# Kernel optimization log

Hardware: AMD Instinct MI355X
Metric: run time of the kernel (lower is better)

## Reference

```python
import jax, jax.numpy as jnp
import numpy as np

N = 320
C_Z = 128
H = 4
C_H = 32


def setup_inputs() -> dict:
    key = jax.random.key(0)
    ks = jax.random.split(key, 9)
    s = 0.02
    return {
        "x_normed": jax.random.normal(ks[0], (1, N, N, C_Z), dtype=jnp.float32),
        "triangle_bias": jax.random.normal(ks[1], (1, 1, H, N, N), dtype=jnp.float32),
        "wq": jax.random.normal(ks[2], (C_Z, H * C_H), dtype=jnp.float32) * s,
        "wk": jax.random.normal(ks[3], (C_Z, H * C_H), dtype=jnp.float32) * s,
        "wv": jax.random.normal(ks[4], (C_Z, H * C_H), dtype=jnp.float32) * s,
        "wg": jax.random.normal(ks[5], (C_Z, H * C_H), dtype=jnp.float32) * s,
        "bg": jnp.ones((H * C_H,), dtype=jnp.float32),  # OpenFold gating bias init = 1
        "wo": jax.random.normal(ks[6], (H * C_H, C_Z), dtype=jnp.float32) * s,
        "bo": jnp.zeros((C_Z,), dtype=jnp.float32),
    }


def reference(x_normed, triangle_bias, wq, wk, wv, wg, bg, wo, bo):
    b, n, m, cz = x_normed.shape  # [1, N, N, C_Z]
    # q/k/v projections (no bias, per OpenFold Attention)
    q = (x_normed @ wq).reshape(b, n, m, H, C_H) / np.sqrt(C_H)
    k = (x_normed @ wk).reshape(b, n, m, H, C_H)
    v = (x_normed @ wv).reshape(b, n, m, H, C_H)
    # attention over the last row dim; first N is a batch dim.
    # scores: [b, n, H, q, k]; triangle_bias [1, 1, H, N, N] broadcasts over n.
    scores = jnp.einsum("bnqhc,bnkhc->bnhqk", q, k) + triangle_bias
    a = jax.nn.softmax(scores, axis=-1)
    o = jnp.einsum("bnhqk,bnkhc->bnqhc", a, v)
    # sigmoid output gating
    g = jax.nn.sigmoid((x_normed @ wg + bg).reshape(b, n, m, H, C_H))
    o = o * g
    out = o.reshape(b, n, m, H * C_H) @ wo + bo
    return out
```

## Files before the change

kernel.cpp:

```cpp
#include <hip/hip_runtime.h>

typedef __bf16 bf16;
typedef __bf16 bf16x8 __attribute__((ext_vector_type(8)));
typedef __bf16 bf16x4 __attribute__((ext_vector_type(4)));
typedef __bf16 bf16x2 __attribute__((ext_vector_type(2)));
typedef float  f32x4  __attribute__((ext_vector_type(4)));
typedef unsigned int u32;
typedef u32 u32x4 __attribute__((ext_vector_type(4)));

#define NN_  320
#define CZ_  128
#define H_   4
#define CH_  32
#define LOG2E_ 1.4426950408889634f

__device__ __forceinline__ u32 pack_bf16(float a, float b) {
    bf16x2 t; t[0] = (bf16)a; t[1] = (bf16)b;
    return __builtin_bit_cast(u32, t);
}

__global__ __launch_bounds__(512) void qkvg_kernel(
    const float* __restrict__ x,
    const float* __restrict__ wq, const float* __restrict__ wk,
    const float* __restrict__ wv, const float* __restrict__ wg,
    const float* __restrict__ bg,
    bf16* __restrict__ Qp, bf16* __restrict__ Kp,
    bf16* __restrict__ Vp, bf16* __restrict__ Gp)
{
    __shared__ bf16 wl[128][136];
    const int tid  = threadIdx.x;
    const int lane = tid & 63, wid = tid >> 6;
    const int l15  = lane & 15, l4 = lane >> 4;
    const int m0   = blockIdx.x << 7;

    const int arow = m0 + wid * 16 + l15;
    bf16x8 xf[4];
    #pragma unroll
    for (int ks = 0; ks < 4; ++ks) {
        float4 f0 = *reinterpret_cast<const float4*>(x + (size_t)arow * CZ_ + ks * 32 + l4 * 8);
        float4 f1 = *reinterpret_cast<const float4*>(x + (size_t)arow * CZ_ + ks * 32 + l4 * 8 + 4);
        bf16x8 t;
        t[0]=(bf16)f0.x; t[1]=(bf16)f0.y; t[2]=(bf16)f0.z; t[3]=(bf16)f0.w;
        t[4]=(bf16)f1.x; t[5]=(bf16)f1.y; t[6]=(bf16)f1.z; t[7]=(bf16)f1.w;
        xf[ks] = t;
    }

    int nQ[4], qQ[4];
    #pragma unroll
    for (int r = 0; r < 4; ++r) {
        int m = m0 + wid * 16 + l4 * 4 + r;
        nQ[r] = m / NN_; qQ[r] = m - nQ[r] * NN_;
    }
    const int nV = arow / NN_, qV = arow - nV * NN_;

    const float* Ws[4] = {wq, wk, wv, wg};
    #pragma unroll
    for (int mat = 0; mat < 4; ++mat) {
        __syncthreads();
        const float* w = Ws[mat];
        #pragma unroll
        for (int it = 0; it < 8; ++it) {
            int u  = tid + (it << 9);
            int j  = u & 127, k4 = u >> 7;
            bf16x4 t;
            t[0] = (bf16)w[(k4 * 4 + 0) * CZ_ + j];
            t[1] = (bf16)w[(k4 * 4 + 1) * CZ_ + j];
            t[2] = (bf16)w[(k4 * 4 + 2) * CZ_ + j];
            t[3] = (bf16)w[(k4 * 4 + 3) * CZ_ + j];
            *reinterpret_cast<bf16x4*>(&wl[j][k4 * 4]) = t;
        }
        __syncthreads();

        f32x4 zero = {0.f, 0.f, 0.f, 0.f};
        f32x4 acc[8];
        #pragma unroll
        for (int ct = 0; ct < 8; ++ct) acc[ct] = zero;

        #pragma unroll
        for (int ks = 0; ks < 4; ++ks) {
            #pragma unroll
            for (int ct = 0; ct < 8; ++ct) {
                bf16x8 wf = *reinterpret_cast<const bf16x8*>(&wl[ct * 16 + l15][ks * 32 + l4 * 8]);
                if (mat == 2)
                    acc[ct] = __builtin_amdgcn_mfma_f32_16x16x32_bf16(wf, xf[ks], acc[ct], 0, 0, 0);
                else
                    acc[ct] = __builtin_amdgcn_mfma_f32_16x16x32_bf16(xf[ks], wf, acc[ct], 0, 0, 0);
            }
        }

        if (mat == 0) {
            #pragma unroll
            for (int ct = 0; ct < 8; ++ct) {
                const int cout = ct * 16 + l15, hh = cout >> 5, cc = cout & 31;
                #pragma unroll
                for (int r = 0; r < 4; ++r)
                    Qp[(size_t)((nQ[r] * H_ + hh) * NN_ + qQ[r]) * CH_ + cc] =
                        (bf16)(acc[ct][r] * 0.25500003540695464f);
            }
        } else if (mat == 1) {
            #pragma unroll
            for (int ct = 0; ct < 8; ++ct) {
                const int cout = ct * 16 + l15, hh = cout >> 5, cc = cout & 31;
                #pragma unroll
                for (int r = 0; r < 4; ++r)
                    Kp[(size_t)((nQ[r] * H_ + hh) * NN_ + qQ[r]) * CH_ + cc] = (bf16)acc[ct][r];
            }
        } else if (mat == 2) {
            #pragma unroll
            for (int ct = 0; ct < 8; ++ct) {
                #pragma unroll
                for (int r = 0; r < 4; ++r) {
                    const int cout = ct * 16 + l4 * 4 + r, hh = cout >> 5, cc = cout & 31;
                    Vp[(size_t)((nV * H_ + hh) * CH_ + cc) * NN_ + qV] = (bf16)acc[ct][r];
                }
            }
        } else {
            #pragma unroll
            for (int ct = 0; ct < 8; ++ct) {
                const int cout = ct * 16 + l15;
                const float bgj = bg[cout];
                #pragma unroll
                for (int r = 0; r < 4; ++r) {
                    float t = acc[ct][r] + bgj;
                    Gp[(size_t)(m0 + wid * 16 + l4 * 4 + r) * CZ_ + cout] =
                        (bf16)(1.0f / (1.0f + __expf(-t)));
                }
            }
        }
    }
}

__global__ __launch_bounds__(640, 3) void attn_kernel(
    const bf16* __restrict__ Qp, const bf16* __restrict__ Kp,
    const bf16* __restrict__ Vp, bf16* __restrict__ Gp,
    const float* __restrict__ bias)
{
    __shared__ bf16 Kl[320][40];
    __shared__ bf16 Vl[32][328];
    const int tid  = threadIdx.x;
    const int lane = tid & 63;
    const int wid  = tid >> 6;
    const int l15  = lane & 15, l4 = lane >> 4;
    const int gid = blockIdx.x;
    const int lin = (gid & 7) * 160 + (gid >> 3);
    const int h   = lin / NN_;
    const int n   = lin - h * NN_;

    const size_t nh = (size_t)(n * H_ + h);
    const bf16* Kh = Kp + nh * NN_ * CH_;
    const bf16* Vh = Vp + nh * CH_ * NN_;
    const bf16* Qh = Qp + nh * NN_ * CH_;

    #pragma unroll
    for (int i = 0; i < 2; ++i) {
        int c  = tid + i * 640;
        int kr = c >> 2, kc = (c & 3) * 8;
        *reinterpret_cast<bf16x8*>(&Kl[kr][kc]) =
            *reinterpret_cast<const bf16x8*>(Kh + kr * CH_ + kc);
        int vr = c / 40, vc = c - vr * 40;
        int m = vc & 3, b32 = vc >> 2;
        bf16x8 g = *reinterpret_cast<const bf16x8*>(Vh + vr * NN_ + vc * 8);
        int base = b32 * 32 + (m & 1) * 16 + (m >> 1) * 4;
        bf16x4 lo; lo[0] = g[0]; lo[1] = g[1]; lo[2] = g[2]; lo[3] = g[3];
        bf16x4 hi; hi[0] = g[4]; hi[1] = g[5]; hi[2] = g[6]; hi[3] = g[7];
        *reinterpret_cast<bf16x4*>(&Vl[vr][base]) = lo;
        *reinterpret_cast<bf16x4*>(&Vl[vr][base + 8]) = hi;
    }
    __syncthreads();

    const f32x4 zero = {0.f, 0.f, 0.f, 0.f};
    bf16x8 onesf;
    #pragma unroll
    for (int i = 0; i < 8; ++i) onesf[i] = (bf16)1.0f;

    const int qbq[2] = {wid * 32, wid * 32 + 16};
    bf16x8 qf[2];
    const float* bq[2];
    size_t gbase[2];
    bf16x4 g0[2], g1[2];
    f32x4 o0[2], o1[2], ol[2];
    float4 bA0[2], bA1[2], bB0[2], bB1[2];

    #pragma unroll
    for (int qg = 0; qg < 2; ++qg) {
        const int qb = qbq[qg];
        qf[qg] = *reinterpret_cast<const bf16x8*>(&Qh[(qb + l15) * CH_ + l4 * 8]);
        bq[qg] = bias + ((size_t)h * NN_ + qb + l15) * NN_ + l4 * 4;
        gbase[qg] = ((size_t)n * NN_ + qb + l15) * CZ_ + h * CH_;
        g0[qg] = *reinterpret_cast<const bf16x4*>(&Gp[gbase[qg] + l4 * 4]);
        g1[qg] = *reinterpret_cast<const bf16x4*>(&Gp[gbase[qg] + 16 + l4 * 4]);
        o0[qg] = zero; o1[qg] = zero; ol[qg] = zero;
        bA0[qg] = *reinterpret_cast<const float4*>(bq[qg]);
        bA1[qg] = *reinterpret_cast<const float4*>(bq[qg] + 16);
        bB0[qg] = *reinterpret_cast<const float4*>(bq[qg] + 32);
        bB1[qg] = *reinterpret_cast<const float4*>(bq[qg] + 48);
    }

#define ATTN_TP(TP, B0, B1, PRE)                                                   \
    {                                                                              \
        const int kvm = (TP) * 32;                                                 \
        bf16x8 kf0 = *reinterpret_cast<const bf16x8*>(&Kl[kvm + l15][l4 * 8]);     \
        bf16x8 kf1 = *reinterpret_cast<const bf16x8*>(&Kl[kvm + 16 + l15][l4 * 8]);\
        bf16x8 vf0 = *reinterpret_cast<const bf16x8*>(&Vl[l15][kvm + l4 * 8]);     \
        bf16x8 vf1 = *reinterpret_cast<const bf16x8*>(&Vl[16 + l15][kvm + l4 * 8]);\
        f32x4 s0[2], s1[2];                                                        \
        __builtin_amdgcn_s_setprio(1);                                             \
        s0[0] = __builtin_amdgcn_mfma_f32_16x16x32_bf16(kf0, qf[0], zero, 0, 0, 0);\
        s1[0] = __builtin_amdgcn_mfma_f32_16x16x32_bf16(kf1, qf[0], zero, 0, 0, 0);\
        s0[1] = __builtin_amdgcn_mfma_f32_16x16x32_bf16(kf0, qf[1], zero, 0, 0, 0);\
        s1[1] = __builtin_amdgcn_mfma_f32_16x16x32_bf16(kf1, qf[1], zero, 0, 0, 0);\
        __builtin_amdgcn_s_setprio(0);                                             \
        _Pragma("unroll")                                                          \
        for (int qg = 0; qg < 2; ++qg) {                                           \
            float p0 = __builtin_amdgcn_exp2f(__builtin_fmaf(B0[qg].x, LOG2E_, s0[qg][0])); \
            float p1 = __builtin_amdgcn_exp2f(__builtin_fmaf(B0[qg].y, LOG2E_, s0[qg][1])); \
            float p2 = __builtin_amdgcn_exp2f(__builtin_fmaf(B0[qg].z, LOG2E_, s0[qg][2])); \
            float p3 = __builtin_amdgcn_exp2f(__builtin_fmaf(B0[qg].w, LOG2E_, s0[qg][3])); \
            float p4 = __builtin_amdgcn_exp2f(__builtin_fmaf(B1[qg].x, LOG2E_, s1[qg][0])); \
            float p5 = __builtin_amdgcn_exp2f(__builtin_fmaf(B1[qg].y, LOG2E_, s1[qg][1])); \
            float p6 = __builtin_amdgcn_exp2f(__builtin_fmaf(B1[qg].z, LOG2E_, s1[qg][2])); \
            float p7 = __builtin_amdgcn_exp2f(__builtin_fmaf(B1[qg].w, LOG2E_, s1[qg][3])); \
            u32x4 ww;                                                              \
            ww[0] = pack_bf16(p0, p1); ww[1] = pack_bf16(p2, p3);                  \
            ww[2] = pack_bf16(p4, p5); ww[3] = pack_bf16(p6, p7);                  \
            bf16x8 pf = __builtin_bit_cast(bf16x8, ww);                            \
            if (PRE) {                                        \
                B0[qg] = *reinterpret_cast<const float4*>(bq[qg] + ((TP) + 2) * 32);      \
                B1[qg] = *reinterpret_cast<const float4*>(bq[qg] + ((TP) + 2) * 32 + 16); \
            }                                                                      \
            __builtin_amdgcn_s_setprio(1);                                         \
            ol[qg] = __builtin_amdgcn_mfma_f32_16x16x32_bf16(onesf, pf, ol[qg], 0, 0, 0); \
            o0[qg] = __builtin_amdgcn_mfma_f32_16x16x32_bf16(vf0, pf, o0[qg], 0, 0, 0);   \
            o1[qg] = __builtin_amdgcn_mfma_f32_16x16x32_bf16(vf1, pf, o1[qg], 0, 0, 0);   \
            __builtin_amdgcn_s_setprio(0);                                         \
        }                                                                          \
    }

    #pragma unroll 1
    for (int t2 = 0; t2 < 4; ++t2) {
        ATTN_TP(2 * t2,     bA0, bA1, true);
        ATTN_TP(2 * t2 + 1, bB0, bB1, true);
    }
    ATTN_TP(8, bA0, bA1, false);
    ATTN_TP(9, bB0, bB1, false);
#undef ATTN_TP

    #pragma unroll
    for (int qg = 0; qg < 2; ++qg) {
        const float linv = 1.0f / ol[qg][0];
        bf16x4 h0, h1;
        #pragma unroll
        for (int r = 0; r < 4; ++r) {
            h0[r] = (bf16)(o0[qg][r] * linv * (float)g0[qg][r]);
            h1[r] = (bf16)(o1[qg][r] * linv * (float)g1[qg][r]);
        }
        *reinterpret_cast<bf16x4*>(&Gp[gbase[qg] + l4 * 4]) = h0;
        *reinterpret_cast<bf16x4*>(&Gp[gbase[qg] + 16 + l4 * 4]) = h1;
    }
}

__global__ __launch_bounds__(512) void oproj_kernel(
    const bf16* __restrict__ og, const float* __restrict__ wo,
    const float* __restrict__ bo, float* __restrict__ out)
{
    __shared__ bf16 wl[128][136];
    const int tid  = threadIdx.x;
    const int lane = tid & 63, wid = tid >> 6;
    const int l15  = lane & 15, l4 = lane >> 4;
    const int m0   = blockIdx.x << 7;

    #pragma unroll
    for (int it = 0; it < 8; ++it) {
        int u  = tid + (it << 9);
        int j  = u & 127, k4 = u >> 7;
        bf16x4 t;
        t[0] = (bf16)wo[(k4 * 4 + 0) * CZ_ + j];
        t[1] = (bf16)wo[(k4 * 4 + 1) * CZ_ + j];
        t[2] = (bf16)wo[(k4 * 4 + 2) * CZ_ + j];
        t[3] = (bf16)wo[(k4 * 4 + 3) * CZ_ + j];
        *reinterpret_cast<bf16x4*>(&wl[j][k4 * 4]) = t;
    }
    __syncthreads();

    const int arow = m0 + wid * 16 + l15;
    bf16x8 af[4];
    #pragma unroll
    for (int ks = 0; ks < 4; ++ks)
        af[ks] = *reinterpret_cast<const bf16x8*>(&og[(size_t)arow * CZ_ + ks * 32 + l4 * 8]);

    f32x4 zero = {0.f, 0.f, 0.f, 0.f};
    f32x4 acc[8];
    #pragma unroll
    for (int ct = 0; ct < 8; ++ct) acc[ct] = zero;
    #pragma unroll
    for (int ks = 0; ks < 4; ++ks)
        #pragma unroll
        for (int ct = 0; ct < 8; ++ct) {
            bf16x8 wf = *reinterpret_cast<const bf16x8*>(&wl[ct * 16 + l15][ks * 32 + l4 * 8]);
            acc[ct] = __builtin_amdgcn_mfma_f32_16x16x32_bf16(af[ks], wf, acc[ct], 0, 0, 0);
        }

    #pragma unroll
    for (int ct = 0; ct < 8; ++ct) {
        const int cout = ct * 16 + l15;
        const float bov = bo[cout];
        #pragma unroll
        for (int r = 0; r < 4; ++r)
            out[(size_t)(m0 + wid * 16 + l4 * 4 + r) * CZ_ + cout] = acc[ct][r] + bov;
    }
}

extern "C" void kernel_launch(void* const* d_in, const int* in_sizes, int n_in,
                              void* d_out, int out_size, void* d_ws, size_t ws_size,
                              hipStream_t stream) {
    (void)in_sizes; (void)n_in; (void)out_size; (void)ws_size;
    const float* x    = (const float*)d_in[0];
    const float* bias = (const float*)d_in[1];
    const float* wq   = (const float*)d_in[2];
    const float* wk   = (const float*)d_in[3];
    const float* wv   = (const float*)d_in[4];
    const float* wg   = (const float*)d_in[5];
    const float* bg   = (const float*)d_in[6];
    const float* wo   = (const float*)d_in[7];
    const float* bo   = (const float*)d_in[8];
    float* out = (float*)d_out;

    const size_t ELEMS = (size_t)NN_ * NN_ * CZ_;
    bf16* Qp = (bf16*)d_ws;
    bf16* Gp = Qp + ELEMS;
    bf16* Kp = (bf16*)d_out;
    bf16* Vp = Kp + ELEMS;

    qkvg_kernel<<<dim3(800), 512, 0, stream>>>(x, wq, wk, wv, wg, bg, Qp, Kp, Vp, Gp);
    attn_kernel<<<dim3(1280), 640, 0, stream>>>(Qp, Kp, Vp, Gp, bias);
    oproj_kernel<<<dim3(800), 512, 0, stream>>>(Gp, wo, bo, out);
}
```

Before: 140.2 us.

## Split attention KV range across warps, prefetch weights, halve oproj grid

The attention kernel now runs each (n,h) with two blocks, each covering half the query rows. Inside a block, warps split the key range into two halves, and the partial outputs and row sums are combined through shared memory before gating. The qkvg kernel prefetches the next weight matrix into registers while the current one is used, overlapping global loads with MFMA work. The oproj kernel processes two row tiles per block so the weight conversion is amortised. This raises parallelism and overlap at the cost of more K/V reloading per (n,h), an extra reduction with barriers, and higher register pressure.

Result: slower. 149.8 us (+6.9%).

```diff
diff --git a/kernel.cpp b/kernel.cpp
--- a/kernel.cpp
+++ b/kernel.cpp
@@ -54,22 +54,37 @@
     const int nV = arow / NN_, qV = arow - nV * NN_;
 
     const float* Ws[4] = {wq, wk, wv, wg};
+
+    float pw[8][4];
+    #pragma unroll
+    for (int it = 0; it < 8; ++it) {
+        const int u = tid + (it << 9), j = u & 127, k4 = u >> 7;
+        #pragma unroll
+        for (int r = 0; r < 4; ++r) pw[it][r] = wq[(k4 * 4 + r) * CZ_ + j];
+    }
+
     #pragma unroll
     for (int mat = 0; mat < 4; ++mat) {
         __syncthreads();
-        const float* w = Ws[mat];
         #pragma unroll
         for (int it = 0; it < 8; ++it) {
-            int u  = tid + (it << 9);
-            int j  = u & 127, k4 = u >> 7;
+            const int u = tid + (it << 9), j = u & 127, k4 = u >> 7;
             bf16x4 t;
-            t[0] = (bf16)w[(k4 * 4 + 0) * CZ_ + j];
-            t[1] = (bf16)w[(k4 * 4 + 1) * CZ_ + j];
-            t[2] = (bf16)w[(k4 * 4 + 2) * CZ_ + j];
-            t[3] = (bf16)w[(k4 * 4 + 3) * CZ_ + j];
+            t[0] = (bf16)pw[it][0]; t[1] = (bf16)pw[it][1];
+            t[2] = (bf16)pw[it][2]; t[3] = (bf16)pw[it][3];
             *reinterpret_cast<bf16x4*>(&wl[j][k4 * 4]) = t;
         }
         __syncthreads();
+
+        if (mat < 3) {
+            const float* wnext = Ws[mat + 1];
+            #pragma unroll
+            for (int it = 0; it < 8; ++it) {
+                const int u = tid + (it << 9), j = u & 127, k4 = u >> 7;
+                #pragma unroll
+                for (int r = 0; r < 4; ++r) pw[it][r] = wnext[(k4 * 4 + r) * CZ_ + j];
+            }
+        }
 
         f32x4 zero = {0.f, 0.f, 0.f, 0.f};
         f32x4 acc[8];
@@ -135,16 +150,21 @@
     const bf16* __restrict__ Vp, bf16* __restrict__ Gp,
     const float* __restrict__ bias)
 {
-    __shared__ bf16 Kl[320][40];
-    __shared__ bf16 Vl[32][328];
+    __shared__ __align__(16) bf16 smem[23296];
+    bf16 (*Kl)[40]  = reinterpret_cast<bf16(*)[40]>(smem);
+    bf16 (*Vl)[328] = reinterpret_cast<bf16(*)[328]>(smem + 12800);
     const int tid  = threadIdx.x;
     const int lane = tid & 63;
     const int wid  = tid >> 6;
     const int l15  = lane & 15, l4 = lane >> 4;
-    const int gid = blockIdx.x;
-    const int lin = (gid & 7) * 160 + (gid >> 3);
-    const int h   = lin / NN_;
-    const int n   = lin - h * NN_;
+    const int gid  = blockIdx.x;
+    const int lin  = (gid & 7) * 320 + (gid >> 3);
+    const int h    = lin / 640;
+    const int rem  = lin - h * 640;
+    const int n    = rem >> 1;
+    const int half = rem & 1;
+    const int qt   = wid % 5;
+    const int kvh  = wid / 5;
 
     const size_t nh = (size_t)(n * H_ + h);
     const bf16* Kh = Kp + nh * NN_ * CH_;
@@ -173,22 +193,18 @@
     #pragma unroll
     for (int i = 0; i < 8; ++i) onesf[i] = (bf16)1.0f;
 
-    const int qbq[2] = {wid * 32, wid * 32 + 16};
+    const int qb0 = half * 160 + qt * 32;
+    const int kvb = kvh * 160;
     bf16x8 qf[2];
     const float* bq[2];
-    size_t gbase[2];
-    bf16x4 g0[2], g1[2];
     f32x4 o0[2], o1[2], ol[2];
     float4 bA0[2], bA1[2], bB0[2], bB1[2];
 
     #pragma unroll
     for (int qg = 0; qg < 2; ++qg) {
-        const int qb = qbq[qg];
+        const int qb = qb0 + qg * 16;
         qf[qg] = *reinterpret_cast<const bf16x8*>(&Qh[(qb + l15) * CH_ + l4 * 8]);
-        bq[qg] = bias + ((size_t)h * NN_ + qb + l15) * NN_ + l4 * 4;
-        gbase[qg] = ((size_t)n * NN_ + qb + l15) * CZ_ + h * CH_;
-        g0[qg] = *reinterpret_cast<const bf16x4*>(&Gp[gbase[qg] + l4 * 4]);
-        g1[qg] = *reinterpret_cast<const bf16x4*>(&Gp[gbase[qg] + 16 + l4 * 4]);
+        bq[qg] = bias + ((size_t)h * NN_ + qb + l15) * NN_ + kvb + l4 * 4;
         o0[qg] = zero; o1[qg] = zero; ol[qg] = zero;
         bA0[qg] = *reinterpret_cast<const float4*>(bq[qg]);
         bA1[qg] = *reinterpret_cast<const float4*>(bq[qg] + 16);
@@ -198,7 +214,7 @@
 
 #define ATTN_TP(TP, B0, B1, PRE)                                                   \
     {                                                                              \
-        const int kvm = (TP) * 32;                                                 \
+        const int kvm = kvb + (TP) * 32;                                           \
         bf16x8 kf0 = *reinterpret_cast<const bf16x8*>(&Kl[kvm + l15][l4 * 8]);     \
         bf16x8 kf1 = *reinterpret_cast<const bf16x8*>(&Kl[kvm + 16 + l15][l4 * 8]);\
         bf16x8 vf0 = *reinterpret_cast<const bf16x8*>(&Vl[l15][kvm + l4 * 8]);     \
@@ -224,7 +240,7 @@
             ww[0] = pack_bf16(p0, p1); ww[1] = pack_bf16(p2, p3);                  \
             ww[2] = pack_bf16(p4, p5); ww[3] = pack_bf16(p6, p7);                  \
             bf16x8 pf = __builtin_bit_cast(bf16x8, ww);                            \
-            if (PRE) {                                        \
+            if (PRE) {            \
                 B0[qg] = *reinterpret_cast<const float4*>(bq[qg] + ((TP) + 2) * 32);      \
                 B1[qg] = *reinterpret_cast<const float4*>(bq[qg] + ((TP) + 2) * 32 + 16); \
             }                                                                      \
@@ -236,26 +252,48 @@
         }                                                                          \
     }
 
-    #pragma unroll 1
-    for (int t2 = 0; t2 < 4; ++t2) {
-        ATTN_TP(2 * t2,     bA0, bA1, true);
-        ATTN_TP(2 * t2 + 1, bB0, bB1, true);
-    }
-    ATTN_TP(8, bA0, bA1, false);
-    ATTN_TP(9, bB0, bB1, false);
+    ATTN_TP(0, bA0, bA1, true);
+    ATTN_TP(1, bB0, bB1, true);
+    ATTN_TP(2, bA0, bA1, true);
+    ATTN_TP(3, bB0, bB1, false);
+    ATTN_TP(4, bA0, bA1, false);
 #undef ATTN_TP
 
-    #pragma unroll
-    for (int qg = 0; qg < 2; ++qg) {
-        const float linv = 1.0f / ol[qg][0];
-        bf16x4 h0, h1;
-        #pragma unroll
-        for (int r = 0; r < 4; ++r) {
-            h0[r] = (bf16)(o0[qg][r] * linv * (float)g0[qg][r]);
-            h1[r] = (bf16)(o1[qg][r] * linv * (float)g1[qg][r]);
-        }
-        *reinterpret_cast<bf16x4*>(&Gp[gbase[qg] + l4 * 4]) = h0;
-        *reinterpret_cast<bf16x4*>(&Gp[gbase[qg] + 16 + l4 * 4]) = h1;
+    __syncthreads();
+    float* red = reinterpret_cast<float*>(smem);
+    float* p = red + (size_t)(qt * 64 + lane) * 20;
+    if (kvh == 1) {
+        *reinterpret_cast<f32x4*>(p)      = o0[0];
+        *reinterpret_cast<f32x4*>(p + 4)  = o1[0];
+        *reinterpret_cast<f32x4*>(p + 8)  = o0[1];
+        *reinterpret_cast<f32x4*>(p + 12) = o1[1];
+        p[16] = ol[0][0];
+        p[17] = ol[1][0];
+    }
+    __syncthreads();
+    if (kvh == 0) {
+        o0[0] += *reinterpret_cast<const f32x4*>(p);
+        o1[0] += *reinterpret_cast<const f32x4*>(p + 4);
+        o0[1] += *reinterpret_cast<const f32x4*>(p + 8);
+        o1[1] += *reinterpret_cast<const f32x4*>(p + 12);
+        const float l0 = ol[0][0] + p[16];
+        const float l1 = ol[1][0] + p[17];
+        #pragma unroll
+        for (int qg = 0; qg < 2; ++qg) {
+            const int qb = qb0 + qg * 16;
+            const size_t gbase = ((size_t)n * NN_ + qb + l15) * CZ_ + h * CH_;
+            const bf16x4 g0 = *reinterpret_cast<const bf16x4*>(&Gp[gbase + l4 * 4]);
+            const bf16x4 g1 = *reinterpret_cast<const bf16x4*>(&Gp[gbase + 16 + l4 * 4]);
+            const float linv = 1.0f / (qg ? l1 : l0);
+            bf16x4 h0, h1;
+            #pragma unroll
+            for (int r = 0; r < 4; ++r) {
+                h0[r] = (bf16)(o0[qg][r] * linv * (float)g0[r]);
+                h1[r] = (bf16)(o1[qg][r] * linv * (float)g1[r]);
+            }
+            *reinterpret_cast<bf16x4*>(&Gp[gbase + l4 * 4]) = h0;
+            *reinterpret_cast<bf16x4*>(&Gp[gbase + 16 + l4 * 4]) = h1;
+        }
     }
 }
 
@@ -267,7 +305,6 @@
     const int tid  = threadIdx.x;
     const int lane = tid & 63, wid = tid >> 6;
     const int l15  = lane & 15, l4 = lane >> 4;
-    const int m0   = blockIdx.x << 7;
 
     #pragma unroll
     for (int it = 0; it < 8; ++it) {
@@ -282,31 +319,35 @@
     }
     __syncthreads();
 
-    const int arow = m0 + wid * 16 + l15;
-    bf16x8 af[4];
-    #pragma unroll
-    for (int ks = 0; ks < 4; ++ks)
-        af[ks] = *reinterpret_cast<const bf16x8*>(&og[(size_t)arow * CZ_ + ks * 32 + l4 * 8]);
-
-    f32x4 zero = {0.f, 0.f, 0.f, 0.f};
-    f32x4 acc[8];
-    #pragma unroll
-    for (int ct = 0; ct < 8; ++ct) acc[ct] = zero;
-    #pragma unroll
-    for (int ks = 0; ks < 4; ++ks)
+    #pragma unroll 1
+    for (int rt = 0; rt < 2; ++rt) {
+        const int m0 = (blockIdx.x << 8) + rt * 128;
+        const int arow = m0 + wid * 16 + l15;
+        bf16x8 af[4];
+        #pragma unroll
+        for (int ks = 0; ks < 4; ++ks)
+            af[ks] = *reinterpret_cast<const bf16x8*>(&og[(size_t)arow * CZ_ + ks * 32 + l4 * 8]);
+
+        f32x4 zero = {0.f, 0.f, 0.f, 0.f};
+        f32x4 acc[8];
+        #pragma unroll
+        for (int ct = 0; ct < 8; ++ct) acc[ct] = zero;
+        #pragma unroll
+        for (int ks = 0; ks < 4; ++ks)
+            #pragma unroll
+            for (int ct = 0; ct < 8; ++ct) {
+                bf16x8 wf = *reinterpret_cast<const bf16x8*>(&wl[ct * 16 + l15][ks * 32 + l4 * 8]);
+                acc[ct] = __builtin_amdgcn_mfma_f32_16x16x32_bf16(af[ks], wf, acc[ct], 0, 0, 0);
+            }
+
         #pragma unroll
         for (int ct = 0; ct < 8; ++ct) {
-            bf16x8 wf = *reinterpret_cast<const bf16x8*>(&wl[ct * 16 + l15][ks * 32 + l4 * 8]);
-            acc[ct] = __builtin_amdgcn_mfma_f32_16x16x32_bf16(af[ks], wf, acc[ct], 0, 0, 0);
-        }
-
-    #pragma unroll
-    for (int ct = 0; ct < 8; ++ct) {
-        const int cout = ct * 16 + l15;
-        const float bov = bo[cout];
-        #pragma unroll
-        for (int r = 0; r < 4; ++r)
-            out[(size_t)(m0 + wid * 16 + l4 * 4 + r) * CZ_ + cout] = acc[ct][r] + bov;
+            const int cout = ct * 16 + l15;
+            const float bov = bo[cout];
+            #pragma unroll
+            for (int r = 0; r < 4; ++r)
+                out[(size_t)(m0 + wid * 16 + l4 * 4 + r) * CZ_ + cout] = acc[ct][r] + bov;
+        }
     }
 }
 
@@ -332,6 +373,6 @@
     bf16* Vp = Kp + ELEMS;
 
     qkvg_kernel<<<dim3(800), 512, 0, stream>>>(x, wq, wk, wv, wg, bg, Qp, Kp, Vp, Gp);
-    attn_kernel<<<dim3(1280), 640, 0, stream>>>(Qp, Kp, Vp, Gp, bias);
-    oproj_kernel<<<dim3(800), 512, 0, stream>>>(Gp, wo, bo, out);
-}
+    attn_kernel<<<dim3(2560), 640, 0, stream>>>(Qp, Kp, Vp, Gp, bias);
+    oproj_kernel<<<dim3(400), 512, 0, stream>>>(Gp, wo, bo, out);
+}
```

## Stage QKVG outputs through LDS for coalesced stores, prefetch weights, halve oproj grid

Applied to the files above, without the earlier changes.

The QKVG projection now writes each output tile into a shared-memory buffer and then stores it to global memory as 16-byte vectors. This replaces the scattered 2-byte stores, including the transposed V layout. It also prefetches the next weight matrix into registers while the MFMAs run, and drops the s_setprio hints from the attention loop. The output-projection kernel processes two 128-row tiles per block, so each block's weight conversion is reused across twice as many rows. The trade-offs are an extra barrier and more LDS in QKVG, higher register pressure, and less parallelism in oproj.

New measurement: 149.2 us. +6.4%, slower.

```diff
diff --git a/kernel.cpp b/kernel.cpp
--- a/kernel.cpp
+++ b/kernel.cpp
@@ -28,6 +28,7 @@
     bf16* __restrict__ Vp, bf16* __restrict__ Gp)
 {
     __shared__ bf16 wl[128][136];
+    __shared__ bf16 sb[128][132];
     const int tid  = threadIdx.x;
     const int lane = tid & 63, wid = tid >> 6;
     const int l15  = lane & 15, l4 = lane >> 4;
@@ -45,31 +46,38 @@
         xf[ks] = t;
     }
 
-    int nQ[4], qQ[4];
-    #pragma unroll
-    for (int r = 0; r < 4; ++r) {
-        int m = m0 + wid * 16 + l4 * 4 + r;
-        nQ[r] = m / NN_; qQ[r] = m - nQ[r] * NN_;
-    }
-    const int nV = arow / NN_, qV = arow - nV * NN_;
-
     const float* Ws[4] = {wq, wk, wv, wg};
+
+    float pw[8][4];
+    #pragma unroll
+    for (int it = 0; it < 8; ++it) {
+        const int u = tid + (it << 9), j = u & 127, k4 = u >> 7;
+        #pragma unroll
+        for (int r = 0; r < 4; ++r) pw[it][r] = wq[(k4 * 4 + r) * CZ_ + j];
+    }
+
     #pragma unroll
     for (int mat = 0; mat < 4; ++mat) {
         __syncthreads();
-        const float* w = Ws[mat];
         #pragma unroll
         for (int it = 0; it < 8; ++it) {
-            int u  = tid + (it << 9);
-            int j  = u & 127, k4 = u >> 7;
+            const int u = tid + (it << 9), j = u & 127, k4 = u >> 7;
             bf16x4 t;
-            t[0] = (bf16)w[(k4 * 4 + 0) * CZ_ + j];
-            t[1] = (bf16)w[(k4 * 4 + 1) * CZ_ + j];
-            t[2] = (bf16)w[(k4 * 4 + 2) * CZ_ + j];
-            t[3] = (bf16)w[(k4 * 4 + 3) * CZ_ + j];
+            t[0] = (bf16)pw[it][0]; t[1] = (bf16)pw[it][1];
+            t[2] = (bf16)pw[it][2]; t[3] = (bf16)pw[it][3];
             *reinterpret_cast<bf16x4*>(&wl[j][k4 * 4]) = t;
         }
         __syncthreads();
+
+        if (mat < 3) {
+            const float* wnext = Ws[mat + 1];
+            #pragma unroll
+            for (int it = 0; it < 8; ++it) {
+                const int u = tid + (it << 9), j = u & 127, k4 = u >> 7;
+                #pragma unroll
+                for (int r = 0; r < 4; ++r) pw[it][r] = wnext[(k4 * 4 + r) * CZ_ + j];
+            }
+        }
 
         f32x4 zero = {0.f, 0.f, 0.f, 0.f};
         f32x4 acc[8];
@@ -90,41 +98,54 @@
 
         if (mat == 0) {
             #pragma unroll
+            for (int ct = 0; ct < 8; ++ct)
+                #pragma unroll
+                for (int r = 0; r < 4; ++r)
+                    sb[wid * 16 + l4 * 4 + r][ct * 16 + l15] =
+                        (bf16)(acc[ct][r] * 0.25500003540695464f);
+        } else if (mat == 1) {
+            #pragma unroll
+            for (int ct = 0; ct < 8; ++ct)
+                #pragma unroll
+                for (int r = 0; r < 4; ++r)
+                    sb[wid * 16 + l4 * 4 + r][ct * 16 + l15] = (bf16)acc[ct][r];
+        } else if (mat == 2) {
+            #pragma unroll
+            for (int ct = 0; ct < 8; ++ct)
+                #pragma unroll
+                for (int r = 0; r < 4; ++r)
+                    sb[ct * 16 + l4 * 4 + r][wid * 16 + l15] = (bf16)acc[ct][r];
+        } else {
+            #pragma unroll
             for (int ct = 0; ct < 8; ++ct) {
-                const int cout = ct * 16 + l15, hh = cout >> 5, cc = cout & 31;
-                #pragma unroll
-                for (int r = 0; r < 4; ++r)
-                    Qp[(size_t)((nQ[r] * H_ + hh) * NN_ + qQ[r]) * CH_ + cc] =
-                        (bf16)(acc[ct][r] * 0.25500003540695464f);
-            }
-        } else if (mat == 1) {
-            #pragma unroll
-            for (int ct = 0; ct < 8; ++ct) {
-                const int cout = ct * 16 + l15, hh = cout >> 5, cc = cout & 31;
-                #pragma unroll
-                for (int r = 0; r < 4; ++r)
-                    Kp[(size_t)((nQ[r] * H_ + hh) * NN_ + qQ[r]) * CH_ + cc] = (bf16)acc[ct][r];
-            }
-        } else if (mat == 2) {
-            #pragma unroll
-            for (int ct = 0; ct < 8; ++ct) {
-                #pragma unroll
-                for (int r = 0; r < 4; ++r) {
-                    const int cout = ct * 16 + l4 * 4 + r, hh = cout >> 5, cc = cout & 31;
-                    Vp[(size_t)((nV * H_ + hh) * CH_ + cc) * NN_ + qV] = (bf16)acc[ct][r];
-                }
-            }
-        } else {
-            #pragma unroll
-            for (int ct = 0; ct < 8; ++ct) {
-                const int cout = ct * 16 + l15;
-                const float bgj = bg[cout];
+                const float bgj = bg[ct * 16 + l15];
                 #pragma unroll
                 for (int r = 0; r < 4; ++r) {
                     float t = acc[ct][r] + bgj;
-                    Gp[(size_t)(m0 + wid * 16 + l4 * 4 + r) * CZ_ + cout] =
+                    sb[wid * 16 + l4 * 4 + r][ct * 16 + l15] =
                         (bf16)(1.0f / (1.0f + __expf(-t)));
                 }
+            }
+        }
+        __syncthreads();
+
+        #pragma unroll
+        for (int i = 0; i < 4; ++i) {
+            const int c   = tid + (i << 9);
+            const int row = c >> 4, ck = c & 15;
+            bf16x8 v = *reinterpret_cast<const bf16x8*>(&sb[row][ck * 8]);
+            if (mat == 0 || mat == 1) {
+                const int m = m0 + row, nn2 = m / NN_, qq2 = m - nn2 * NN_;
+                bf16* dst = (mat == 0) ? Qp : Kp;
+                *reinterpret_cast<bf16x8*>(
+                    &dst[((size_t)(nn2 * H_ + (ck >> 2)) * NN_ + qq2) * CH_ + (ck & 3) * 8]) = v;
+            } else if (mat == 2) {
+                const int mg = m0 + ck * 8;
+                const int nn2 = mg / NN_, qq2 = mg - nn2 * NN_;
+                *reinterpret_cast<bf16x8*>(
+                    &Vp[((size_t)(nn2 * H_ + (row >> 5)) * CH_ + (row & 31)) * NN_ + qq2]) = v;
+            } else {
+                *reinterpret_cast<bf16x8*>(&Gp[(size_t)(m0 + row) * CZ_ + ck * 8]) = v;
             }
         }
     }
@@ -204,12 +225,10 @@
         bf16x8 vf0 = *reinterpret_cast<const bf16x8*>(&Vl[l15][kvm + l4 * 8]);     \
         bf16x8 vf1 = *reinterpret_cast<const bf16x8*>(&Vl[16 + l15][kvm + l4 * 8]);\
         f32x4 s0[2], s1[2];                                                        \
-        __builtin_amdgcn_s_setprio(1);                                             \
         s0[0] = __builtin_amdgcn_mfma_f32_16x16x32_bf16(kf0, qf[0], zero, 0, 0, 0);\
         s1[0] = __builtin_amdgcn_mfma_f32_16x16x32_bf16(kf1, qf[0], zero, 0, 0, 0);\
         s0[1] = __builtin_amdgcn_mfma_f32_16x16x32_bf16(kf0, qf[1], zero, 0, 0, 0);\
         s1[1] = __builtin_amdgcn_mfma_f32_16x16x32_bf16(kf1, qf[1], zero, 0, 0, 0);\
-        __builtin_amdgcn_s_setprio(0);                                             \
         _Pragma("unroll")                                                          \
         for (int qg = 0; qg < 2; ++qg) {                                           \
             float p0 = __builtin_amdgcn_exp2f(__builtin_fmaf(B0[qg].x, LOG2E_, s0[qg][0])); \
@@ -228,11 +247,9 @@
                 B0[qg] = *reinterpret_cast<const float4*>(bq[qg] + ((TP) + 2) * 32);      \
                 B1[qg] = *reinterpret_cast<const float4*>(bq[qg] + ((TP) + 2) * 32 + 16); \
             }                                                                      \
-            __builtin_amdgcn_s_setprio(1);                                         \
             ol[qg] = __builtin_amdgcn_mfma_f32_16x16x32_bf16(onesf, pf, ol[qg], 0, 0, 0); \
             o0[qg] = __builtin_amdgcn_mfma_f32_16x16x32_bf16(vf0, pf, o0[qg], 0, 0, 0);   \
             o1[qg] = __builtin_amdgcn_mfma_f32_16x16x32_bf16(vf1, pf, o1[qg], 0, 0, 0);   \
-            __builtin_amdgcn_s_setprio(0);                                         \
         }                                                                          \
     }
 
@@ -267,7 +284,6 @@
     const int tid  = threadIdx.x;
     const int lane = tid & 63, wid = tid >> 6;
     const int l15  = lane & 15, l4 = lane >> 4;
-    const int m0   = blockIdx.x << 7;
 
     #pragma unroll
     for (int it = 0; it < 8; ++it) {
@@ -282,31 +298,35 @@
     }
     __syncthreads();
 
-    const int arow = m0 + wid * 16 + l15;
-    bf16x8 af[4];
-    #pragma unroll
-    for (int ks = 0; ks < 4; ++ks)
-        af[ks] = *reinterpret_cast<const bf16x8*>(&og[(size_t)arow * CZ_ + ks * 32 + l4 * 8]);
-
-    f32x4 zero = {0.f, 0.f, 0.f, 0.f};
-    f32x4 acc[8];
-    #pragma unroll
-    for (int ct = 0; ct < 8; ++ct) acc[ct] = zero;
-    #pragma unroll
-    for (int ks = 0; ks < 4; ++ks)
+    #pragma unroll 1
+    for (int rt = 0; rt < 2; ++rt) {
+        const int m0 = (blockIdx.x << 8) + rt * 128;
+        const int arow = m0 + wid * 16 + l15;
+        bf16x8 af[4];
+        #pragma unroll
+        for (int ks = 0; ks < 4; ++ks)
+            af[ks] = *reinterpret_cast<const bf16x8*>(&og[(size_t)arow * CZ_ + ks * 32 + l4 * 8]);
+
+        f32x4 zero = {0.f, 0.f, 0.f, 0.f};
+        f32x4 acc[8];
+        #pragma unroll
+        for (int ct = 0; ct < 8; ++ct) acc[ct] = zero;
+        #pragma unroll
+        for (int ks = 0; ks < 4; ++ks)
+            #pragma unroll
+            for (int ct = 0; ct < 8; ++ct) {
+                bf16x8 wf = *reinterpret_cast<const bf16x8*>(&wl[ct * 16 + l15][ks * 32 + l4 * 8]);
+                acc[ct] = __builtin_amdgcn_mfma_f32_16x16x32_bf16(af[ks], wf, acc[ct], 0, 0, 0);
+            }
+
         #pragma unroll
         for (int ct = 0; ct < 8; ++ct) {
-            bf16x8 wf = *reinterpret_cast<const bf16x8*>(&wl[ct * 16 + l15][ks * 32 + l4 * 8]);
-            acc[ct] = __builtin_amdgcn_mfma_f32_16x16x32_bf16(af[ks], wf, acc[ct], 0, 0, 0);
-        }
-
-    #pragma unroll
-    for (int ct = 0; ct < 8; ++ct) {
-        const int cout = ct * 16 + l15;
-        const float bov = bo[cout];
-        #pragma unroll
-        for (int r = 0; r < 4; ++r)
-            out[(size_t)(m0 + wid * 16 + l4 * 4 + r) * CZ_ + cout] = acc[ct][r] + bov;
+            const int cout = ct * 16 + l15;
+            const float bov = bo[cout];
+            #pragma unroll
+            for (int r = 0; r < 4; ++r)
+                out[(size_t)(m0 + wid * 16 + l4 * 4 + r) * CZ_ + cout] = acc[ct][r] + bov;
+        }
     }
 }
 
@@ -333,5 +353,5 @@
 
     qkvg_kernel<<<dim3(800), 512, 0, stream>>>(x, wq, wk, wv, wg, bg, Qp, Kp, Vp, Gp);
     attn_kernel<<<dim3(1280), 640, 0, stream>>>(Qp, Kp, Vp, Gp, bias);
-    oproj_kernel<<<dim3(800), 512, 0, stream>>>(Gp, wo, bo, out);
-}
+    oproj_kernel<<<dim3(400), 512, 0, stream>>>(Gp, wo, bo, out);
+}
```
